# Performance work log

Hardware: AMD Instinct MI355X
Metric: run time of the kernel (lower is better)

Reference implementation:

```python
import jax, jax.numpy as jnp
import numpy as np

SEQ, BATCH = 256, 8
N_NODES = SEQ * BATCH
VOCAB, D_MODEL, H, D_K, D_FF, N_LAYERS, MAX_POS = 259, 256, 8, 32, 1024, 2, 128


def setup_inputs() -> dict:
    key = jax.random.key(0)
    ks = jax.random.split(key, 16)
    # structured causal edge list per sequence (dst attends to src <= dst, incl. self)
    tri_dst, tri_src = np.tril_indices(SEQ)
    offs = (np.arange(BATCH) * SEQ)[:, None]
    edge_src = jnp.asarray((tri_src[None, :] + offs).ravel(), dtype=jnp.int64)
    edge_dst = jnp.asarray((tri_dst[None, :] + offs).ravel(), dtype=jnp.int64)
    positions = jnp.tile(jnp.arange(SEQ, dtype=jnp.int64), BATCH)
    tokens = jax.random.randint(ks[0], (N_NODES,), 0, VOCAB, dtype=jnp.int64)
    s = 0.02
    p = lambda k, shp: jax.random.normal(k, shp, dtype=jnp.float32) * s
    return {
        "tokens": tokens, "positions": positions,
        "edge_src": edge_src, "edge_dst": edge_dst,
        "coord_emb": p(ks[1], (3, D_MODEL)),
        "pos_emb": p(ks[2], (MAX_POS, D_MODEL)),
        "value_emb": p(ks[3], (VOCAB, D_MODEL)),
        "ln1_scale": jnp.ones((N_LAYERS, D_MODEL)), "ln1_bias": jnp.zeros((N_LAYERS, D_MODEL)),
        "Wqkv": p(ks[4], (N_LAYERS, D_MODEL, 3 * D_MODEL)),
        "Wo": p(ks[5], (N_LAYERS, D_MODEL, D_MODEL)),
        "ln2_scale": jnp.ones((N_LAYERS, D_MODEL)), "ln2_bias": jnp.zeros((N_LAYERS, D_MODEL)),
        "W1": p(ks[6], (N_LAYERS, D_MODEL, D_FF)), "b1": jnp.zeros((N_LAYERS, D_FF)),
        "W2": p(ks[7], (N_LAYERS, D_FF, D_MODEL)), "b2": jnp.zeros((N_LAYERS, D_MODEL)),
        "lnf_scale": jnp.ones((D_MODEL,)), "lnf_bias": jnp.zeros((D_MODEL,)),
        "Wg": p(ks[8], (D_MODEL, VOCAB)), "bg": jnp.zeros((VOCAB,)),
    }


def _ln(x, scale, bias, eps=1e-5):
    mu = jnp.mean(x, axis=-1, keepdims=True)
    var = jnp.var(x, axis=-1, keepdims=True)
    return (x - mu) * jax.lax.rsqrt(var + eps) * scale + bias


def _graph_attention(x, src, dst, Wqkv, Wo, ln_s, ln_b):
    n = x.shape[0]
    xn = _ln(x, ln_s, ln_b)
    qkv = (xn @ Wqkv).reshape(n, 3, H, D_K)
    q, k, v = qkv[:, 0], qkv[:, 1], qkv[:, 2]  # [n, H, D_K] each
    # u_dot_v('k','q','score') per edge, scaled
    score = jnp.einsum("ehd,ehd->eh", k[src], q[dst]) / jnp.sqrt(jnp.float32(D_K))
    # edge_softmax over incoming edges of each dst node
    smax = jax.ops.segment_max(score, dst, num_segments=n)      # [n, H]
    ex = jnp.exp(score - smax[dst])                              # [E, H]
    denom = jax.ops.segment_sum(ex, dst, num_segments=n)        # [n, H]
    alpha = ex / denom[dst]
    # u_mul_e('v','softmax_score') + sum reduce -> z on dst nodes
    z = jax.ops.segment_sum(alpha[:, :, None] * v[src], dst, num_segments=n)  # [n, H, D_K]
    return x + z.reshape(n, D_MODEL) @ Wo


def reference(tokens, positions, edge_src, edge_dst, coord_emb, pos_emb, value_emb,
              ln1_scale, ln1_bias, Wqkv, Wo, ln2_scale, ln2_bias, W1, b1, W2, b2,
              lnf_scale, lnf_bias, Wg, bg):
    x = coord_emb[positions % 3] + pos_emb[positions // 3] + value_emb[tokens]
    for i in range(Wqkv.shape[0]):
        x = _graph_attention(x, edge_src, edge_dst, Wqkv[i], Wo[i], ln1_scale[i], ln1_bias[i])
        h = _ln(x, ln2_scale[i], ln2_bias[i])
        x = x + jax.nn.relu(h @ W1[i] + b1[i]) @ W2[i] + b2[i]
    out = _ln(x, lnf_scale, lnf_bias) @ Wg + bg
    return jax.nn.log_softmax(out, axis=-1)
```

## Files before the change

kernel.cpp:

```cpp
#include <hip/hip_runtime.h>
#include <hip/hip_bf16.h>

typedef __hip_bfloat16 bf16;
typedef unsigned short ushort_t;
typedef unsigned int uint_t;
typedef __attribute__((ext_vector_type(8))) short short8;
typedef __attribute__((ext_vector_type(4))) float floatx4;

#define D_MODEL 256
#define SEQ     256
#define BATCH   8
#define NN      2048
#define NHEAD   8
#define DK      32
#define DFF     1024
#define VOCAB   259
#define NLAYER  2

#define WQKVT_OFF 0
#define WOT_OFF   393216
#define W1T_OFF   524288
#define W2T_OFF   1048576
#define WGT_OFF   1572864
#define WT_TOTAL  1639168
// ... 178 lines not shown
    int base = b * SEQ;
    int dstBase = tile * 64;
    int tileEnd = (tile + 1) * 64;

    int nV = tileEnd * 4;
    for (int i = t; i < nV; i += 256) {
        int src = i >> 2, g = i & 3;
        const ushort_t* rp = qkvB + (size_t)(base + src) * 768 + h * 32 + g * 8;
        uint4 kv = *reinterpret_cast<const uint4*>(rp + 256);
        *reinterpret_cast<uint4*>(&u.a.Ks[src][g * 8]) = kv;
        uint4 vv = *reinterpret_cast<const uint4*>(rp + 512);
        const ushort_t* vs = (const ushort_t*)&vv;
        #pragma unroll
        for (int j = 0; j < 8; ++j) Vt[g * 8 + j][src] = vs[j];
    }
    {
        int r = t >> 2, g = t & 3;
        uint4 qv = *reinterpret_cast<const uint4*>(
            qkvB + (size_t)(base + dstBase + r) * 768 + h * 32 + g * 8);
        *reinterpret_cast<uint4*>(&u.a.Qs[r][g * 8]) = qv;
    }
    __syncthreads();

    const float scale = 0.17677669529663687f;
    int stLim = tile * 4 + wave;
    int stCnt = stLim + 1;
    short8 qf = *reinterpret_cast<const short8*>(&u.a.Qs[wave * 16 + l16][quad * 8]);
    floatx4 accs[16];
    #pragma unroll
    for (int st = 0; st < 16; ++st) {
        if (st <= stLim) {
            short8 kf = *reinterpret_cast<const short8*>(&u.a.Ks[st * 16 + l16][quad * 8]);
            accs[st] = __builtin_amdgcn_mfma_f32_16x16x32_bf16(qf, kf, (floatx4){0.f,0.f,0.f,0.f}, 0, 0, 0);
        }
    }
    float mrow[4] = {-3e38f, -3e38f, -3e38f, -3e38f};
    #pragma unroll
    for (int st = 0; st < 16; ++st) {
        if (st <= stLim) {
            int srcg = st * 16 + l16;
            #pragma unroll
            for (int r = 0; r < 4; ++r) {
                int dstg = dstBase + wave * 16 + quad * 4 + r;
                float sv = (srcg <= dstg) ? accs[st][r] * scale : -3e38f;
                accs[st][r] = sv;
                mrow[r] = fmaxf(mrow[r], sv);
            }
        }
    }
    #pragma unroll
    for (int mk = 1; mk < 16; mk <<= 1)
        #pragma unroll
        for (int r = 0; r < 4; ++r) mrow[r] = fmaxf(mrow[r], __shfl_xor(mrow[r], mk, 64));
    float lrow[4] = {0.f, 0.f, 0.f, 0.f};
    #pragma unroll
    for (int st = 0; st < 16; ++st) {
        if (st <= stLim) {
            #pragma unroll
            for (int r = 0; r < 4; ++r) {
                float p = __expf(accs[st][r] - mrow[r]);
                accs[st][r] = p;
                lrow[r] += p;
            }
        }
    }
    #pragma unroll
    for (int mk = 1; mk < 16; mk <<= 1)
        #pragma unroll
        for (int r = 0; r < 4; ++r) lrow[r] += __shfl_xor(lrow[r], mk, 64);
    __syncthreads();

    #pragma unroll
    for (int st = 0; st < 16; ++st) {
        if (st <= stLim) {
            #pragma unroll
            for (int r = 0; r < 4; ++r)
                u.Ps[wave * 16 + quad * 4 + r][st * 16 + l16] = f2bs(accs[st][r]);
        }
    }
    if (stCnt & 1) {
        #pragma unroll
        for (int r = 0; r < 4; ++r)
            u.Ps[wave * 16 + quad * 4 + r][stCnt * 16 + l16] = 0;
    }
    __syncthreads();

    int ktCnt = (stCnt + 1) >> 1;
    floatx4 acco[2];
    acco[0] = (floatx4){0.f,0.f,0.f,0.f};
    acco[1] = (floatx4){0.f,0.f,0.f,0.f};
    #pragma unroll
    for (int kt = 0; kt < 8; ++kt) {
        if (kt < ktCnt) {
            short8 pf = *reinterpret_cast<const short8*>(&u.Ps[wave * 16 + l16][kt * 32 + quad * 8]);
            #pragma unroll
            for (int dn = 0; dn < 2; ++dn) {
                short8 vf = *reinterpret_cast<const short8*>(&Vt[dn * 16 + l16][kt * 32 + quad * 8]);
                acco[dn] = __builtin_amdgcn_mfma_f32_16x16x32_bf16(pf, vf, acco[dn], 0, 0, 0);
            }
        }
    }
    #pragma unroll
    for (int dn = 0; dn < 2; ++dn)
        #pragma unroll
        for (int r = 0; r < 4; ++r)
            zB[(size_t)(base + dstBase + wave * 16 + quad * 4 + r) * 256
               + h * 32 + dn * 16 + l16] = f2bs(acco[dn][r] / lrow[r]);
}

__global__ void __launch_bounds__(256) gemm_k(const ushort_t* __restrict__ A, int K,
        const ushort_t* __restrict__ BT, const float* __restrict__ bias,
        ushort_t* __restrict__ C, int ldc, int relu) {
    int t = threadIdx.x;
    int lane = t & 63, wave = t >> 6;
    int quad = lane >> 4, l16 = lane & 15;
    int wm = (wave >> 1) * 32, wn = (wave & 1) * 32;
    int rowBase = blockIdx.x * 64, colBase = blockIdx.y * 64;
    floatx4 acc[2][2];
    #pragma unroll
    for (int a = 0; a < 2; ++a)
        #pragma unroll
        for (int b = 0; b < 2; ++b) acc[a][b] = (floatx4){0.f,0.f,0.f,0.f};
    const ushort_t* a0 = A + (size_t)(rowBase + wm + l16) * K + quad * 8;
    const ushort_t* a1 = a0 + (size_t)16 * K;
    const ushort_t* b0 = BT + (size_t)(colBase + wn + l16) * K + quad * 8;
    const ushort_t* b1 = b0 + (size_t)16 * K;
    #pragma unroll 8
    for (int k0 = 0; k0 < K; k0 += 32) {
        short8 af0 = *reinterpret_cast<const short8*>(a0 + k0);
        short8 af1 = *reinterpret_cast<const short8*>(a1 + k0);
        short8 bf0 = *reinterpret_cast<const short8*>(b0 + k0);
        short8 bf1 = *reinterpret_cast<const short8*>(b1 + k0);
        acc[0][0] = __builtin_amdgcn_mfma_f32_16x16x32_bf16(af0, bf0, acc[0][0], 0,0,0);
        acc[0][1] = __builtin_amdgcn_mfma_f32_16x16x32_bf16(af0, bf1, acc[0][1], 0,0,0);
        acc[1][0] = __builtin_amdgcn_mfma_f32_16x16x32_bf16(af1, bf0, acc[1][0], 0,0,0);
        acc[1][1] = __builtin_amdgcn_mfma_f32_16x16x32_bf16(af1, bf1, acc[1][1], 0,0,0);
    }
    #pragma unroll
    for (int nt = 0; nt < 2; ++nt) {
        int col = colBase + wn + nt*16 + l16;
        float bb = bias ? bias[col] : 0.f;
        #pragma unroll
        for (int mt = 0; mt < 2; ++mt)
            #pragma unroll
            for (int r = 0; r < 4; ++r) {
                int row = rowBase + wm + mt*16 + quad*4 + r;
                float v = acc[mt][nt][r] + bb;
                if (relu) v = fmaxf(v, 0.f);
                C[(size_t)row * ldc + col] = f2bs(v);
            }
    }
}

union TailHU {
    ushort_t hmid[16][1032];
    float    Lg[16][273];
};

__device__ __forceinline__ void ln16_store(const float (*xrow)[256],
        const float* __restrict__ ls, const float* __restrict__ lb,
        ushort_t (*xnA)[264]) {
    int lane = threadIdx.x & 63, wave = threadIdx.x >> 6;
    #pragma unroll
    for (int i = 0; i < 4; ++i) {
        int row = wave*4 + i, c0 = lane * 4;
        float4 vv = *reinterpret_cast<const float4*>(&xrow[row][c0]);
        float s  = wred_sum(vv.x + vv.y + vv.z + vv.w);
        float s2 = wred_sum(vv.x*vv.x + vv.y*vv.y + vv.z*vv.z + vv.w*vv.w);
        float mu = s * (1.f/256.f);
        float var = s2 * (1.f/256.f) - mu*mu;
        float rstd = rsqrtf(var + 1e-5f);
        ushort4 o;
        o.x = f2bs((vv.x-mu)*rstd*ls[c0+0] + lb[c0+0]);
        o.y = f2bs((vv.y-mu)*rstd*ls[c0+1] + lb[c0+1]);
        o.z = f2bs((vv.z-mu)*rstd*ls[c0+2] + lb[c0+2]);
        o.w = f2bs((vv.w-mu)*rstd*ls[c0+3] + lb[c0+3]);
        *reinterpret_cast<ushort4*>(&xnA[row][c0]) = o;
    }
}

__global__ void __launch_bounds__(256) tail_k(
        const ushort_t* __restrict__ zB,
        const ushort_t* __restrict__ WoT,
        float* __restrict__ x,
        const float* __restrict__ ls2, const float* __restrict__ lb2,
        const ushort_t* __restrict__ W1T, const float* __restrict__ b1P,
        const ushort_t* __restrict__ W2T, const float* __restrict__ b2P,
        const float* __restrict__ lsN, const float* __restrict__ lbN,
        const ushort_t* __restrict__ WqkvTn, ushort_t* __restrict__ qkvB,
        const ushort_t* __restrict__ WgT, const float* __restrict__ bgP,
        const void* __restrict__ ln1sRaw, void* __restrict__ outp, int doLogits) {
    __shared__ ushort_t xnA[16][264];
    __shared__ float    xrow[16][256];
    __shared__ TailHU   hu;
    int t = threadIdx.x, lane = t & 63, wave = t >> 6;
    int quad = lane >> 4, l16 = lane & 15;
    int rowBase = blockIdx.x * 16;
    int cb = wave * 64;
    float vpre[4][4];

    {
        floatx4 acc[4];
        #pragma unroll
        for (int nt = 0; nt < 4; ++nt) acc[nt] = (floatx4){0.f,0.f,0.f,0.f};
        const ushort_t* a0 = zB + (size_t)(rowBase + l16) * 256 + quad * 8;
        #pragma unroll
        for (int k0 = 0; k0 < 256; k0 += 32) {
            short8 af = *reinterpret_cast<const short8*>(a0 + k0);
            #pragma unroll
            for (int nt = 0; nt < 4; ++nt) {
                short8 bv = *reinterpret_cast<const short8*>(
                    WoT + (size_t)(cb + nt*16 + l16) * 256 + k0 + quad * 8);
                acc[nt] = __builtin_amdgcn_mfma_f32_16x16x32_bf16(af, bv, acc[nt], 0,0,0);
            }
        }
        #pragma unroll
        for (int nt = 0; nt < 4; ++nt) {
            int col = cb + nt*16 + l16;
            #pragma unroll
            for (int r = 0; r < 4; ++r) {
                int row = quad*4 + r;
                float v = acc[nt][r] + x[(size_t)(rowBase + row) * 256 + col];
                vpre[nt][r] = v;
                xrow[row][col] = v;
            }
        }
    }
    __syncthreads();
    ln16_store(xrow, ls2, lb2, xnA);
    __syncthreads();

    {
        floatx4 acc[16];
        #pragma unroll
        for (int nt = 0; nt < 16; ++nt) acc[nt] = (floatx4){0.f,0.f,0.f,0.f};
        const ushort_t* a0 = &xnA[l16][quad * 8];
        #pragma unroll
        for (int k0 = 0; k0 < 256; k0 += 32) {
            short8 af = *reinterpret_cast<const short8*>(a0 + k0);
            #pragma unroll
            for (int nt = 0; nt < 16; ++nt) {
                short8 bv = *reinterpret_cast<const short8*>(
                    W1T + (size_t)(wave*256 + nt*16 + l16) * 256 + k0 + quad * 8);
                acc[nt] = __builtin_amdgcn_mfma_f32_16x16x32_bf16(af, bv, acc[nt], 0,0,0);
            }
        }
        #pragma unroll
        for (int nt = 0; nt < 16; ++nt) {
            int col = wave*256 + nt*16 + l16;
            float bb = b1P[col];
            #pragma unroll
            for (int r = 0; r < 4; ++r)
                hu.hmid[quad*4 + r][col] = f2bs(fmaxf(acc[nt][r] + bb, 0.f));
        }
    }
    __syncthreads();

    {
        floatx4 acc[4];
        #pragma unroll
        for (int nt = 0; nt < 4; ++nt) acc[nt] = (floatx4){0.f,0.f,0.f,0.f};
        #pragma unroll 8
        for (int k0 = 0; k0 < 1024; k0 += 32) {
            short8 af = *reinterpret_cast<const short8*>(&hu.hmid[l16][k0 + quad * 8]);
            #pragma unroll
            for (int nt = 0; nt < 4; ++nt) {
                short8 bv = *reinterpret_cast<const short8*>(
                    W2T + (size_t)(cb + nt*16 + l16) * 1024 + k0 + quad * 8);
                acc[nt] = __builtin_amdgcn_mfma_f32_16x16x32_bf16(af, bv, acc[nt], 0,0,0);
            }
        }
        #pragma unroll
        for (int nt = 0; nt < 4; ++nt) {
            int col = cb + nt*16 + l16;
            float bb = b2P[col];
            #pragma unroll
            for (int r = 0; r < 4; ++r) {
                int row = quad*4 + r;
                float v = acc[nt][r] + bb + vpre[nt][r];
                x[(size_t)(rowBase + row) * 256 + col] = v;
                xrow[row][col] = v;
            }
        }
    }
    __syncthreads();
    ln16_store(xrow, lsN, lbN, xnA);
    __syncthreads();

    if (WqkvTn) {
        floatx4 acc[12];
        #pragma unroll
        for (int nt = 0; nt < 12; ++nt) acc[nt] = (floatx4){0.f,0.f,0.f,0.f};
        const ushort_t* a0 = &xnA[l16][quad * 8];
        #pragma unroll
        for (int k0 = 0; k0 < 256; k0 += 32) {
            short8 af = *reinterpret_cast<const short8*>(a0 + k0);
            #pragma unroll
            for (int nt = 0; nt < 12; ++nt) {
                short8 bv = *reinterpret_cast<const short8*>(
                    WqkvTn + (size_t)(wave*192 + nt*16 + l16) * 256 + k0 + quad * 8);
                acc[nt] = __builtin_amdgcn_mfma_f32_16x16x32_bf16(af, bv, acc[nt], 0,0,0);
            }
        }
        #pragma unroll
        for (int nt = 0; nt < 12; ++nt) {
            int col = wave*192 + nt*16 + l16;
            #pragma unroll
            for (int r = 0; r < 4; ++r)
                qkvB[(size_t)(rowBase + quad*4 + r) * 768 + col] = f2bs(acc[nt][r]);
        }
    }

    if (doLogits) {
        const ushort_t* a0 = &xnA[l16][quad * 8];
        {
            floatx4 acc[4];
            #pragma unroll
            for (int nt = 0; nt < 4; ++nt) acc[nt] = (floatx4){0.f,0.f,0.f,0.f};
            #pragma unroll
            for (int kc = 0; kc < 8; ++kc) {
                short8 af = *reinterpret_cast<const short8*>(a0 + kc * 32);
                #pragma unroll
                for (int nt = 0; nt < 4; ++nt) {
                    short8 bv = *reinterpret_cast<const short8*>(
                        WgT + (size_t)(cb + nt*16 + l16) * 256 + kc*32 + quad*8);
                    acc[nt] = __builtin_amdgcn_mfma_f32_16x16x32_bf16(af, bv, acc[nt], 0,0,0);
                }
            }
            #pragma unroll
            for (int nt = 0; nt < 4; ++nt) {
                int col = cb + nt*16 + l16;
                float bb = bgP[col];
                #pragma unroll
                for (int r = 0; r < 4; ++r)
                    hu.Lg[quad*4 + r][col] = acc[nt][r] + bb;
            }
        }
        if (wave == 0) {
            floatx4 acc = (floatx4){0.f,0.f,0.f,0.f};
            int n = 256 + l16;
            int nc = (n < VOCAB) ? n : 0;
            const ushort_t* b0 = WgT + (size_t)nc * 256 + quad * 8;
            #pragma unroll
            for (int kc = 0; kc < 8; ++kc) {
                short8 af = *reinterpret_cast<const short8*>(a0 + kc * 32);
                short8 bv = *reinterpret_cast<const short8*>(b0 + kc * 32);
                acc = __builtin_amdgcn_mfma_f32_16x16x32_bf16(af, bv, acc, 0,0,0);
            }
            #pragma unroll
            for (int r = 0; r < 4; ++r)
                hu.Lg[quad*4 + r][256 + l16] = (n < VOCAB) ? (acc[r] + bgP[n]) : -1e30f;
        }
        __syncthreads();
        int outBF = detBF(ln1sRaw) ? 1 : 0;
        #pragma unroll
        for (int i = 0; i < 4; ++i) {
            int row = wave*4 + i;
            float v0 = hu.Lg[row][lane],     v1 = hu.Lg[row][lane+64];
            float v2 = hu.Lg[row][lane+128], v3 = hu.Lg[row][lane+192];
            float v4 = (lane < 16) ? hu.Lg[row][256+lane] : -1e30f;
            float m = wred_max(fmaxf(fmaxf(fmaxf(v0,v1), fmaxf(v2,v3)), v4));
            float se = __expf(v0-m) + __expf(v1-m) + __expf(v2-m) + __expf(v3-m)
                     + ((lane < 16) ? __expf(v4-m) : 0.f);
            se = wred_sum(se);
            float lse = m + logf(se);
            size_t nbase = (size_t)(rowBase + row) * VOCAB;
            if (outBF) {
                ushort_t* o = (ushort_t*)outp + nbase;
                o[lane]     = f2bs(v0 - lse);
                o[lane+64]  = f2bs(v1 - lse);
                o[lane+128] = f2bs(v2 - lse);
                o[lane+192] = f2bs(v3 - lse);
                if (lane < 3) o[256+lane] = f2bs(v4 - lse);
            } else {
                float* o = (float*)outp + nbase;
                o[lane]     = v0 - lse;
                o[lane+64]  = v1 - lse;
                o[lane+128] = v2 - lse;
                o[lane+192] = v3 - lse;
                if (lane < 3) o[256+lane] = v4 - lse;
            }
        }
    }
}

extern "C" void kernel_launch(void* const* d_in, const int* in_sizes, int n_in,
                              void* d_out, int out_size, void* d_ws, size_t ws_size,
                              hipStream_t stream) {
    const void* tok  = d_in[0];
    const void* pos  = d_in[1];
    const void* ce   = d_in[4];
    const void* pe   = d_in[5];
    const void* ve   = d_in[6];
    const void* ln1s = d_in[7];
    const void* ln1b = d_in[8];
    const void* Wqkv = d_in[9];
    const void* Wo   = d_in[10];
    const void* ln2s = d_in[11];
    const void* ln2b = d_in[12];
    const void* W1   = d_in[13];
    const void* b1   = d_in[14];
    const void* W2   = d_in[15];
    const void* b2   = d_in[16];
    const void* lnfs = d_in[17];
    const void* lnfb = d_in[18];
    const void* Wg   = d_in[19];
    const void* bg   = d_in[20];

    char* base = (char*)d_ws;
    float*    lnP  = (float*)base;
    float*    bP   = (float*)(base + 10240);
    float*    x    = (float*)(base + 22528);
    ushort_t* xn   = (ushort_t*)(base + 2119680);
    ushort_t* zB   = (ushort_t*)(base + 3168256);
    ushort_t* WT   = (ushort_t*)(base + 8411136);
    ushort_t* qkvB = (ushort_t*)(base + 11689472);

    prep_k<<<554, 256, 0, stream>>>(tok, pos, ce, pe, ve,
        Wqkv, Wo, W1, W2, Wg, ln1s, ln1b, ln2s, ln2b, lnfs, lnfb,
        b1, b2, bg, WT, lnP, bP, x, xn);

    gemm_k<<<dim3(32, 12), 256, 0, stream>>>(xn, 256,
        WT + WQKVT_OFF, nullptr, qkvB, 768, 0);

    attn_k<<<256, 256, 0, stream>>>(qkvB, zB);

    tail_k<<<128, 256, 0, stream>>>(zB,
        WT + WOT_OFF, x, lnP + 1024, lnP + 1536,
        WT + W1T_OFF, bP, WT + W2T_OFF, bP + 2048,
        lnP + 256, lnP + 768,
        WT + WQKVT_OFF + 196608, qkvB,
        WT + WGT_OFF, bP + 2560, ln1s, d_out, 0);

    attn_k<<<256, 256, 0, stream>>>(qkvB, zB);

    tail_k<<<128, 256, 0, stream>>>(zB,
        WT + WOT_OFF + 65536, x, lnP + 1024 + 256, lnP + 1536 + 256,
        WT + W1T_OFF + 262144, bP + 1024, WT + W2T_OFF + 262144, bP + 2048 + 256,
        lnP + 2048, lnP + 2304,
        nullptr, qkvB,
        WT + WGT_OFF, bP + 2560, ln1s, d_out, 1);
}
```

Before: 228.6 us.

## Widen tail kernel to 1024 threads, one 16-column tile per wave

The fused tail kernel (Wo projection, LN, FFN, next-layer QKV or logits) goes from 4 waves to 16 waves per 16-row block. Each wave now handles one 16-column output tile instead of four (or a quarter of the previous FFN/QKV columns), and each LN or log-softmax row is handled by one wave. The aim is more waves in flight per block, since only 128 blocks launch and the MFMA chains per wave are long. In exchange, register budget per thread drops under the 1024-thread launch bound, and there is more cross-wave synchronisation per block.

```diff
diff --git a/kernel.cpp b/kernel.cpp
--- a/kernel.cpp
+++ b/kernel.cpp
@@ -362,26 +362,23 @@
 __device__ __forceinline__ void ln16_store(const float (*xrow)[256],
         const float* __restrict__ ls, const float* __restrict__ lb,
         ushort_t (*xnA)[264]) {
-    int lane = threadIdx.x & 63, wave = threadIdx.x >> 6;
-    #pragma unroll
-    for (int i = 0; i < 4; ++i) {
-        int row = wave*4 + i, c0 = lane * 4;
-        float4 vv = *reinterpret_cast<const float4*>(&xrow[row][c0]);
-        float s  = wred_sum(vv.x + vv.y + vv.z + vv.w);
-        float s2 = wred_sum(vv.x*vv.x + vv.y*vv.y + vv.z*vv.z + vv.w*vv.w);
-        float mu = s * (1.f/256.f);
-        float var = s2 * (1.f/256.f) - mu*mu;
-        float rstd = rsqrtf(var + 1e-5f);
-        ushort4 o;
-        o.x = f2bs((vv.x-mu)*rstd*ls[c0+0] + lb[c0+0]);
-        o.y = f2bs((vv.y-mu)*rstd*ls[c0+1] + lb[c0+1]);
-        o.z = f2bs((vv.z-mu)*rstd*ls[c0+2] + lb[c0+2]);
-        o.w = f2bs((vv.w-mu)*rstd*ls[c0+3] + lb[c0+3]);
-        *reinterpret_cast<ushort4*>(&xnA[row][c0]) = o;
-    }
-}
-
-__global__ void __launch_bounds__(256) tail_k(
+    int lane = threadIdx.x & 63, row = threadIdx.x >> 6;
+    int c0 = lane * 4;
+    float4 vv = *reinterpret_cast<const float4*>(&xrow[row][c0]);
+    float s  = wred_sum(vv.x + vv.y + vv.z + vv.w);
+    float s2 = wred_sum(vv.x*vv.x + vv.y*vv.y + vv.z*vv.z + vv.w*vv.w);
+    float mu = s * (1.f/256.f);
+    float var = s2 * (1.f/256.f) - mu*mu;
+    float rstd = rsqrtf(var + 1e-5f);
+    ushort4 o;
+    o.x = f2bs((vv.x-mu)*rstd*ls[c0+0] + lb[c0+0]);
+    o.y = f2bs((vv.y-mu)*rstd*ls[c0+1] + lb[c0+1]);
+    o.z = f2bs((vv.z-mu)*rstd*ls[c0+2] + lb[c0+2]);
+    o.w = f2bs((vv.w-mu)*rstd*ls[c0+3] + lb[c0+3]);
+    *reinterpret_cast<ushort4*>(&xnA[row][c0]) = o;
+}
+
+__global__ void __launch_bounds__(1024) tail_k(
         const ushort_t* __restrict__ zB,
         const ushort_t* __restrict__ WoT,
         float* __restrict__ x,
@@ -398,58 +395,49 @@
     int t = threadIdx.x, lane = t & 63, wave = t >> 6;
     int quad = lane >> 4, l16 = lane & 15;
     int rowBase = blockIdx.x * 16;
-    int cb = wave * 64;
-    float vpre[4][4];
+    float vpre[4];
+
+    {
+        floatx4 acc = (floatx4){0.f,0.f,0.f,0.f};
+        const ushort_t* a0 = zB + (size_t)(rowBase + l16) * 256 + quad * 8;
+        const ushort_t* b0 = WoT + (size_t)(wave*16 + l16) * 256 + quad * 8;
+        #pragma unroll
+        for (int k0 = 0; k0 < 256; k0 += 32) {
+            short8 af = *reinterpret_cast<const short8*>(a0 + k0);
+            short8 bv = *reinterpret_cast<const short8*>(b0 + k0);
+            acc = __builtin_amdgcn_mfma_f32_16x16x32_bf16(af, bv, acc, 0,0,0);
+        }
+        int col = wave*16 + l16;
+        #pragma unroll
+        for (int r = 0; r < 4; ++r) {
+            int row = quad*4 + r;
+            float v = acc[r] + x[(size_t)(rowBase + row) * 256 + col];
+            vpre[r] = v;
+            xrow[row][col] = v;
+        }
+    }
+    __syncthreads();
+    ln16_store(xrow, ls2, lb2, xnA);
+    __syncthreads();
 
     {
         floatx4 acc[4];
         #pragma unroll
         for (int nt = 0; nt < 4; ++nt) acc[nt] = (floatx4){0.f,0.f,0.f,0.f};
-        const ushort_t* a0 = zB + (size_t)(rowBase + l16) * 256 + quad * 8;
+        const ushort_t* a0 = &xnA[l16][quad * 8];
         #pragma unroll
         for (int k0 = 0; k0 < 256; k0 += 32) {
             short8 af = *reinterpret_cast<const short8*>(a0 + k0);
             #pragma unroll
             for (int nt = 0; nt < 4; ++nt) {
                 short8 bv = *reinterpret_cast<const short8*>(
-                    WoT + (size_t)(cb + nt*16 + l16) * 256 + k0 + quad * 8);
+                    W1T + (size_t)(wave*64 + nt*16 + l16) * 256 + k0 + quad * 8);
                 acc[nt] = __builtin_amdgcn_mfma_f32_16x16x32_bf16(af, bv, acc[nt], 0,0,0);
             }
         }
         #pragma unroll
         for (int nt = 0; nt < 4; ++nt) {
-            int col = cb + nt*16 + l16;
-            #pragma unroll
-            for (int r = 0; r < 4; ++r) {
-                int row = quad*4 + r;
-                float v = acc[nt][r] + x[(size_t)(rowBase + row) * 256 + col];
-                vpre[nt][r] = v;
-                xrow[row][col] = v;
-            }
-        }
-    }
-    __syncthreads();
-    ln16_store(xrow, ls2, lb2, xnA);
-    __syncthreads();
-
-    {
-        floatx4 acc[16];
-        #pragma unroll
-        for (int nt = 0; nt < 16; ++nt) acc[nt] = (floatx4){0.f,0.f,0.f,0.f};
-        const ushort_t* a0 = &xnA[l16][quad * 8];
-        #pragma unroll
-        for (int k0 = 0; k0 < 256; k0 += 32) {
-            short8 af = *reinterpret_cast<const short8*>(a0 + k0);
-            #pragma unroll
-            for (int nt = 0; nt < 16; ++nt) {
-                short8 bv = *reinterpret_cast<const short8*>(
-                    W1T + (size_t)(wave*256 + nt*16 + l16) * 256 + k0 + quad * 8);
-                acc[nt] = __builtin_amdgcn_mfma_f32_16x16x32_bf16(af, bv, acc[nt], 0,0,0);
-            }
-        }
-        #pragma unroll
-        for (int nt = 0; nt < 16; ++nt) {
-            int col = wave*256 + nt*16 + l16;
+            int col = wave*64 + nt*16 + l16;
             float bb = b1P[col];
             #pragma unroll
             for (int r = 0; r < 4; ++r)
@@ -459,30 +447,22 @@
     __syncthreads();
 
     {
-        floatx4 acc[4];
-        #pragma unroll
-        for (int nt = 0; nt < 4; ++nt) acc[nt] = (floatx4){0.f,0.f,0.f,0.f};
+        floatx4 acc = (floatx4){0.f,0.f,0.f,0.f};
+        const ushort_t* b0 = W2T + (size_t)(wave*16 + l16) * 1024 + quad * 8;
         #pragma unroll 8
         for (int k0 = 0; k0 < 1024; k0 += 32) {
             short8 af = *reinterpret_cast<const short8*>(&hu.hmid[l16][k0 + quad * 8]);
-            #pragma unroll
-            for (int nt = 0; nt < 4; ++nt) {
-                short8 bv = *reinterpret_cast<const short8*>(
-                    W2T + (size_t)(cb + nt*16 + l16) * 1024 + k0 + quad * 8);
-                acc[nt] = __builtin_amdgcn_mfma_f32_16x16x32_bf16(af, bv, acc[nt], 0,0,0);
-            }
-        }
-        #pragma unroll
-        for (int nt = 0; nt < 4; ++nt) {
-            int col = cb + nt*16 + l16;
-            float bb = b2P[col];
-            #pragma unroll
-            for (int r = 0; r < 4; ++r) {
-                int row = quad*4 + r;
-                float v = acc[nt][r] + bb + vpre[nt][r];
-                x[(size_t)(rowBase + row) * 256 + col] = v;
-                xrow[row][col] = v;
-            }
+            short8 bv = *reinterpret_cast<const short8*>(b0 + k0);
+            acc = __builtin_amdgcn_mfma_f32_16x16x32_bf16(af, bv, acc, 0,0,0);
+        }
+        int col = wave*16 + l16;
+        float bb = b2P[col];
+        #pragma unroll
+        for (int r = 0; r < 4; ++r) {
+            int row = quad*4 + r;
+            float v = acc[r] + bb + vpre[r];
+            x[(size_t)(rowBase + row) * 256 + col] = v;
+            xrow[row][col] = v;
         }
     }
     __syncthreads();
@@ -490,23 +470,23 @@
     __syncthreads();
 
     if (WqkvTn) {
-        floatx4 acc[12];
-        #pragma unroll
-        for (int nt = 0; nt < 12; ++nt) acc[nt] = (floatx4){0.f,0.f,0.f,0.f};
+        floatx4 acc[3];
+        #pragma unroll
+        for (int nt = 0; nt < 3; ++nt) acc[nt] = (floatx4){0.f,0.f,0.f,0.f};
         const ushort_t* a0 = &xnA[l16][quad * 8];
         #pragma unroll
         for (int k0 = 0; k0 < 256; k0 += 32) {
             short8 af = *reinterpret_cast<const short8*>(a0 + k0);
             #pragma unroll
-            for (int nt = 0; nt < 12; ++nt) {
+            for (int nt = 0; nt < 3; ++nt) {
                 short8 bv = *reinterpret_cast<const short8*>(
-                    WqkvTn + (size_t)(wave*192 + nt*16 + l16) * 256 + k0 + quad * 8);
+                    WqkvTn + (size_t)(wave*48 + nt*16 + l16) * 256 + k0 + quad * 8);
                 acc[nt] = __builtin_amdgcn_mfma_f32_16x16x32_bf16(af, bv, acc[nt], 0,0,0);
             }
         }
         #pragma unroll
-        for (int nt = 0; nt < 12; ++nt) {
-            int col = wave*192 + nt*16 + l16;
+        for (int nt = 0; nt < 3; ++nt) {
+            int col = wave*48 + nt*16 + l16;
             #pragma unroll
             for (int r = 0; r < 4; ++r)
                 qkvB[(size_t)(rowBase + quad*4 + r) * 768 + col] = f2bs(acc[nt][r]);
@@ -516,27 +496,19 @@
     if (doLogits) {
         const ushort_t* a0 = &xnA[l16][quad * 8];
         {
-            floatx4 acc[4];
-            #pragma unroll
-            for (int nt = 0; nt < 4; ++nt) acc[nt] = (floatx4){0.f,0.f,0.f,0.f};
+            floatx4 acc = (floatx4){0.f,0.f,0.f,0.f};
+            const ushort_t* b0 = WgT + (size_t)(wave*16 + l16) * 256 + quad * 8;
             #pragma unroll
             for (int kc = 0; kc < 8; ++kc) {
                 short8 af = *reinterpret_cast<const short8*>(a0 + kc * 32);
-                #pragma unroll
-                for (int nt = 0; nt < 4; ++nt) {
-                    short8 bv = *reinterpret_cast<const short8*>(
-                        WgT + (size_t)(cb + nt*16 + l16) * 256 + kc*32 + quad*8);
-                    acc[nt] = __builtin_amdgcn_mfma_f32_16x16x32_bf16(af, bv, acc[nt], 0,0,0);
-                }
-            }
-            #pragma unroll
-            for (int nt = 0; nt < 4; ++nt) {
-                int col = cb + nt*16 + l16;
-                float bb = bgP[col];
-                #pragma unroll
-                for (int r = 0; r < 4; ++r)
-                    hu.Lg[quad*4 + r][col] = acc[nt][r] + bb;
-            }
+                short8 bv = *reinterpret_cast<const short8*>(b0 + kc * 32);
+                acc = __builtin_amdgcn_mfma_f32_16x16x32_bf16(af, bv, acc, 0,0,0);
+            }
+            int col = wave*16 + l16;
+            float bb = bgP[col];
+            #pragma unroll
+            for (int r = 0; r < 4; ++r)
+                hu.Lg[quad*4 + r][col] = acc[r] + bb;
         }
         if (wave == 0) {
             floatx4 acc = (floatx4){0.f,0.f,0.f,0.f};
@@ -555,9 +527,8 @@
         }
         __syncthreads();
         int outBF = detBF(ln1sRaw) ? 1 : 0;
-        #pragma unroll
-        for (int i = 0; i < 4; ++i) {
-            int row = wave*4 + i;
+        {
+            int row = wave;
             float v0 = hu.Lg[row][lane],     v1 = hu.Lg[row][lane+64];
             float v2 = hu.Lg[row][lane+128], v3 = hu.Lg[row][lane+192];
             float v4 = (lane < 16) ? hu.Lg[row][256+lane] : -1e30f;
@@ -627,7 +598,7 @@
 
     attn_k<<<256, 256, 0, stream>>>(qkvB, zB);
 
-    tail_k<<<128, 256, 0, stream>>>(zB,
+    tail_k<<<128, 1024, 0, stream>>>(zB,
         WT + WOT_OFF, x, lnP + 1024, lnP + 1536,
         WT + W1T_OFF, bP, WT + W2T_OFF, bP + 2048,
         lnP + 256, lnP + 768,
@@ -636,7 +607,7 @@
 
     attn_k<<<256, 256, 0, stream>>>(qkvB, zB);
 
-    tail_k<<<128, 256, 0, stream>>>(zB,
+    tail_k<<<128, 1024, 0, stream>>>(zB,
         WT + WOT_OFF + 65536, x, lnP + 1024 + 256, lnP + 1536 + 256,
         WT + W1T_OFF + 262144, bP + 1024, WT + W2T_OFF + 262144, bP + 2048 + 256,
         lnP + 2048, lnP + 2304,
```

New measurement: 229.1 us. About the same (+0.2%).

## Split fused tail kernel into multi-kernel FFN pipeline for more parallelism

Applied to the files above, without the earlier changes.

Replaces the monolithic per-layer tail kernel (128 blocks doing Wo, LN, W1, W2, LN, QKV/logits serially) with four kernels: Wo+LN+W1 on a 64x4 grid, W2 on 64x4, LN+QKV on 32x12, and LN+logits. The goal is to fill the GPU with more blocks, since 128 blocks underuse the CUs. The trade is extra launches, a global round trip for the 2048x1024 hidden activation, and Wo/LN work redone across the 4 column groups. Ping-pong x buffers avoid read/write hazards across blocks.

```diff
diff --git a/kernel.cpp b/kernel.cpp
--- a/kernel.cpp
+++ b/kernel.cpp
@@ -354,19 +354,153 @@
     }
 }
 
-union TailHU {
-    ushort_t hmid[16][1032];
-    float    Lg[16][273];
-};
-
-__device__ __forceinline__ void ln16_store(const float (*xrow)[256],
+__global__ void __launch_bounds__(256) woff1_k(
+        const ushort_t* __restrict__ zB, const ushort_t* __restrict__ WoT,
+        const float* __restrict__ xIn, float* __restrict__ xOut,
+        const float* __restrict__ ls2, const float* __restrict__ lb2,
+        const ushort_t* __restrict__ W1T, const float* __restrict__ b1P,
+        ushort_t* __restrict__ hmidG) {
+    __shared__ float    xrow[32][256];
+    __shared__ ushort_t xnA[32][264];
+    int t = threadIdx.x, lane = t & 63, wave = t >> 6;
+    int quad = lane >> 4, l16 = lane & 15;
+    int rowBase = blockIdx.x * 32, cg = blockIdx.y;
+
+    {
+        floatx4 acc[2][4];
+        #pragma unroll
+        for (int mt = 0; mt < 2; ++mt)
+            #pragma unroll
+            for (int nt = 0; nt < 4; ++nt) acc[mt][nt] = (floatx4){0.f,0.f,0.f,0.f};
+        const ushort_t* a0 = zB + (size_t)(rowBase + l16) * 256 + quad * 8;
+        const ushort_t* a1 = a0 + (size_t)16 * 256;
+        #pragma unroll
+        for (int k0 = 0; k0 < 256; k0 += 32) {
+            short8 af0 = *reinterpret_cast<const short8*>(a0 + k0);
+            short8 af1 = *reinterpret_cast<const short8*>(a1 + k0);
+            #pragma unroll
+            for (int nt = 0; nt < 4; ++nt) {
+                short8 bv = *reinterpret_cast<const short8*>(
+                    WoT + (size_t)(wave*64 + nt*16 + l16) * 256 + k0 + quad * 8);
+                acc[0][nt] = __builtin_amdgcn_mfma_f32_16x16x32_bf16(af0, bv, acc[0][nt], 0,0,0);
+                acc[1][nt] = __builtin_amdgcn_mfma_f32_16x16x32_bf16(af1, bv, acc[1][nt], 0,0,0);
+            }
+        }
+        #pragma unroll
+        for (int nt = 0; nt < 4; ++nt) {
+            int col = wave*64 + nt*16 + l16;
+            #pragma unroll
+            for (int mt = 0; mt < 2; ++mt)
+                #pragma unroll
+                for (int r = 0; r < 4; ++r) {
+                    int row = mt*16 + quad*4 + r;
+                    float v = acc[mt][nt][r] + xIn[(size_t)(rowBase + row) * 256 + col];
+                    xOut[(size_t)(rowBase + row) * 256 + col] = v;
+                    xrow[row][col] = v;
+                }
+        }
+    }
+    __syncthreads();
+    #pragma unroll
+    for (int i = 0; i < 8; ++i) {
+        int row = wave*8 + i, c0 = lane * 4;
+        float4 vv = *reinterpret_cast<const float4*>(&xrow[row][c0]);
+        float s  = wred_sum(vv.x + vv.y + vv.z + vv.w);
+        float s2 = wred_sum(vv.x*vv.x + vv.y*vv.y + vv.z*vv.z + vv.w*vv.w);
+        float mu = s * (1.f/256.f);
+        float var = s2 * (1.f/256.f) - mu*mu;
+        float rstd = rsqrtf(var + 1e-5f);
+        ushort4 o;
+        o.x = f2bs((vv.x-mu)*rstd*ls2[c0+0] + lb2[c0+0]);
+        o.y = f2bs((vv.y-mu)*rstd*ls2[c0+1] + lb2[c0+1]);
+        o.z = f2bs((vv.z-mu)*rstd*ls2[c0+2] + lb2[c0+2]);
+        o.w = f2bs((vv.w-mu)*rstd*ls2[c0+3] + lb2[c0+3]);
+        *reinterpret_cast<ushort4*>(&xnA[row][c0]) = o;
+    }
+    __syncthreads();
+    {
+        floatx4 acc[2][4];
+        #pragma unroll
+        for (int mt = 0; mt < 2; ++mt)
+            #pragma unroll
+            for (int nt = 0; nt < 4; ++nt) acc[mt][nt] = (floatx4){0.f,0.f,0.f,0.f};
+        const ushort_t* a0 = &xnA[l16][quad * 8];
+        const ushort_t* a1 = &xnA[16 + l16][quad * 8];
+        #pragma unroll
+        for (int k0 = 0; k0 < 256; k0 += 32) {
+            short8 af0 = *reinterpret_cast<const short8*>(a0 + k0);
+            short8 af1 = *reinterpret_cast<const short8*>(a1 + k0);
+            #pragma unroll
+            for (int nt = 0; nt < 4; ++nt) {
+                short8 bv = *reinterpret_cast<const short8*>(
+                    W1T + (size_t)(cg*256 + wave*64 + nt*16 + l16) * 256 + k0 + quad * 8);
+                acc[0][nt] = __builtin_amdgcn_mfma_f32_16x16x32_bf16(af0, bv, acc[0][nt], 0,0,0);
+                acc[1][nt] = __builtin_amdgcn_mfma_f32_16x16x32_bf16(af1, bv, acc[1][nt], 0,0,0);
+            }
+        }
+        #pragma unroll
+        for (int nt = 0; nt < 4; ++nt) {
+            int col = cg*256 + wave*64 + nt*16 + l16;
+            float bb = b1P[col];
+            #pragma unroll
+            for (int mt = 0; mt < 2; ++mt)
+                #pragma unroll
+                for (int r = 0; r < 4; ++r) {
+                    int row = mt*16 + quad*4 + r;
+                    hmidG[(size_t)(rowBase + row) * 1024 + col] =
+                        f2bs(fmaxf(acc[mt][nt][r] + bb, 0.f));
+                }
+        }
+    }
+}
+
+__global__ void __launch_bounds__(256) w2_k(
+        const ushort_t* __restrict__ hmidG, const ushort_t* __restrict__ W2T,
+        const float* __restrict__ b2P,
+        const float* __restrict__ xPre, float* __restrict__ yOut) {
+    int t = threadIdx.x, lane = t & 63, wave = t >> 6;
+    int quad = lane >> 4, l16 = lane & 15;
+    int rowBase = blockIdx.x * 32, colBase = blockIdx.y * 64;
+    int wm = (wave >> 1) * 16, wn = (wave & 1) * 32;
+    floatx4 acc[2];
+    acc[0] = (floatx4){0.f,0.f,0.f,0.f};
+    acc[1] = (floatx4){0.f,0.f,0.f,0.f};
+    const ushort_t* a0 = hmidG + (size_t)(rowBase + wm + l16) * 1024 + quad * 8;
+    #pragma unroll 8
+    for (int k0 = 0; k0 < 1024; k0 += 32) {
+        short8 af = *reinterpret_cast<const short8*>(a0 + k0);
+        #pragma unroll
+        for (int nt = 0; nt < 2; ++nt) {
+            short8 bv = *reinterpret_cast<const short8*>(
+                W2T + (size_t)(colBase + wn + nt*16 + l16) * 1024 + k0 + quad * 8);
+            acc[nt] = __builtin_amdgcn_mfma_f32_16x16x32_bf16(af, bv, acc[nt], 0,0,0);
+        }
+    }
+    #pragma unroll
+    for (int nt = 0; nt < 2; ++nt) {
+        int col = colBase + wn + nt*16 + l16;
+        float bb = b2P[col];
+        #pragma unroll
+        for (int r = 0; r < 4; ++r) {
+            int row = wm + quad*4 + r;
+            float v = acc[nt][r] + bb + xPre[(size_t)(rowBase + row) * 256 + col];
+            yOut[(size_t)(rowBase + row) * 256 + col] = v;
+        }
+    }
+}
+
+__global__ void __launch_bounds__(256) lnqkv_k(
+        const float* __restrict__ yIn,
         const float* __restrict__ ls, const float* __restrict__ lb,
-        ushort_t (*xnA)[264]) {
-    int lane = threadIdx.x & 63, wave = threadIdx.x >> 6;
-    #pragma unroll
-    for (int i = 0; i < 4; ++i) {
-        int row = wave*4 + i, c0 = lane * 4;
-        float4 vv = *reinterpret_cast<const float4*>(&xrow[row][c0]);
+        const ushort_t* __restrict__ WqkvT, ushort_t* __restrict__ qkvB) {
+    __shared__ ushort_t xnA[64][264];
+    int t = threadIdx.x, lane = t & 63, wave = t >> 6;
+    int quad = lane >> 4, l16 = lane & 15;
+    int rowBase = blockIdx.x * 64, colBase = blockIdx.y * 64;
+    #pragma unroll
+    for (int i = 0; i < 16; ++i) {
+        int row = wave*16 + i, c0 = lane * 4;
+        float4 vv = *reinterpret_cast<const float4*>(yIn + (size_t)(rowBase + row) * 256 + c0);
         float s  = wred_sum(vv.x + vv.y + vv.z + vv.w);
         float s2 = wred_sum(vv.x*vv.x + vv.y*vv.y + vv.z*vv.z + vv.w*vv.w);
         float mu = s * (1.f/256.f);
@@ -379,209 +513,144 @@
         o.w = f2bs((vv.w-mu)*rstd*ls[c0+3] + lb[c0+3]);
         *reinterpret_cast<ushort4*>(&xnA[row][c0]) = o;
     }
-}
-
-__global__ void __launch_bounds__(256) tail_k(
-        const ushort_t* __restrict__ zB,
-        const ushort_t* __restrict__ WoT,
-        float* __restrict__ x,
-        const float* __restrict__ ls2, const float* __restrict__ lb2,
-        const ushort_t* __restrict__ W1T, const float* __restrict__ b1P,
-        const ushort_t* __restrict__ W2T, const float* __restrict__ b2P,
-        const float* __restrict__ lsN, const float* __restrict__ lbN,
-        const ushort_t* __restrict__ WqkvTn, ushort_t* __restrict__ qkvB,
+    __syncthreads();
+    int wm = (wave >> 1) * 32, wn = (wave & 1) * 32;
+    floatx4 acc[2][2];
+    #pragma unroll
+    for (int a = 0; a < 2; ++a)
+        #pragma unroll
+        for (int b = 0; b < 2; ++b) acc[a][b] = (floatx4){0.f,0.f,0.f,0.f};
+    const ushort_t* a0 = &xnA[wm + l16][quad * 8];
+    const ushort_t* a1 = &xnA[wm + 16 + l16][quad * 8];
+    #pragma unroll
+    for (int k0 = 0; k0 < 256; k0 += 32) {
+        short8 af0 = *reinterpret_cast<const short8*>(a0 + k0);
+        short8 af1 = *reinterpret_cast<const short8*>(a1 + k0);
+        #pragma unroll
+        for (int nt = 0; nt < 2; ++nt) {
+            short8 bv = *reinterpret_cast<const short8*>(
+                WqkvT + (size_t)(colBase + wn + nt*16 + l16) * 256 + k0 + quad * 8);
+            acc[0][nt] = __builtin_amdgcn_mfma_f32_16x16x32_bf16(af0, bv, acc[0][nt], 0,0,0);
+            acc[1][nt] = __builtin_amdgcn_mfma_f32_16x16x32_bf16(af1, bv, acc[1][nt], 0,0,0);
+        }
+    }
+    #pragma unroll
+    for (int nt = 0; nt < 2; ++nt) {
+        int col = colBase + wn + nt*16 + l16;
+        #pragma unroll
+        for (int mt = 0; mt < 2; ++mt)
+            #pragma unroll
+            for (int r = 0; r < 4; ++r) {
+                int row = wm + mt*16 + quad*4 + r;
+                qkvB[(size_t)(rowBase + row) * 768 + col] = f2bs(acc[mt][nt][r]);
+            }
+    }
+}
+
+__global__ void __launch_bounds__(256) lnlg_k(
+        const float* __restrict__ yIn,
+        const float* __restrict__ lnfsP, const float* __restrict__ lnfbP,
         const ushort_t* __restrict__ WgT, const float* __restrict__ bgP,
-        const void* __restrict__ ln1sRaw, void* __restrict__ outp, int doLogits) {
+        const void* __restrict__ ln1sRaw, void* __restrict__ outp) {
+    __shared__ float    xrow[16][256];
     __shared__ ushort_t xnA[16][264];
-    __shared__ float    xrow[16][256];
-    __shared__ TailHU   hu;
+    __shared__ float    Lg[16][273];
     int t = threadIdx.x, lane = t & 63, wave = t >> 6;
     int quad = lane >> 4, l16 = lane & 15;
     int rowBase = blockIdx.x * 16;
+    #pragma unroll
+    for (int i = 0; i < 4; ++i) {
+        int idx = i * 256 + t;
+        int row = idx >> 6, c4 = (idx & 63) * 4;
+        *reinterpret_cast<float4*>(&xrow[row][c4]) =
+            *reinterpret_cast<const float4*>(yIn + (size_t)(rowBase + row) * 256 + c4);
+    }
+    __syncthreads();
+    #pragma unroll
+    for (int i = 0; i < 4; ++i) {
+        int row = wave*4 + i, c0 = lane * 4;
+        float4 vv = *reinterpret_cast<const float4*>(&xrow[row][c0]);
+        float s  = wred_sum(vv.x + vv.y + vv.z + vv.w);
+        float s2 = wred_sum(vv.x*vv.x + vv.y*vv.y + vv.z*vv.z + vv.w*vv.w);
+        float mu = s * (1.f/256.f);
+        float var = s2 * (1.f/256.f) - mu*mu;
+        float rstd = rsqrtf(var + 1e-5f);
+        ushort4 o;
+        o.x = f2bs((vv.x-mu)*rstd*lnfsP[c0+0] + lnfbP[c0+0]);
+        o.y = f2bs((vv.y-mu)*rstd*lnfsP[c0+1] + lnfbP[c0+1]);
+        o.z = f2bs((vv.z-mu)*rstd*lnfsP[c0+2] + lnfbP[c0+2]);
+        o.w = f2bs((vv.w-mu)*rstd*lnfsP[c0+3] + lnfbP[c0+3]);
+        *reinterpret_cast<ushort4*>(&xnA[row][c0]) = o;
+    }
+    __syncthreads();
+    const ushort_t* a0 = &xnA[l16][quad * 8];
     int cb = wave * 64;
-    float vpre[4][4];
-
     {
         floatx4 acc[4];
         #pragma unroll
         for (int nt = 0; nt < 4; ++nt) acc[nt] = (floatx4){0.f,0.f,0.f,0.f};
-        const ushort_t* a0 = zB + (size_t)(rowBase + l16) * 256 + quad * 8;
-        #pragma unroll
-        for (int k0 = 0; k0 < 256; k0 += 32) {
-            short8 af = *reinterpret_cast<const short8*>(a0 + k0);
+        #pragma unroll
+        for (int kc = 0; kc < 8; ++kc) {
+            short8 af = *reinterpret_cast<const short8*>(a0 + kc * 32);
             #pragma unroll
             for (int nt = 0; nt < 4; ++nt) {
                 short8 bv = *reinterpret_cast<const short8*>(
-                    WoT + (size_t)(cb + nt*16 + l16) * 256 + k0 + quad * 8);
+                    WgT + (size_t)(cb + nt*16 + l16) * 256 + kc*32 + quad*8);
                 acc[nt] = __builtin_amdgcn_mfma_f32_16x16x32_bf16(af, bv, acc[nt], 0,0,0);
             }
         }
         #pragma unroll
         for (int nt = 0; nt < 4; ++nt) {
             int col = cb + nt*16 + l16;
-            #pragma unroll
-            for (int r = 0; r < 4; ++r) {
-                int row = quad*4 + r;
-                float v = acc[nt][r] + x[(size_t)(rowBase + row) * 256 + col];
-                vpre[nt][r] = v;
-                xrow[row][col] = v;
-            }
-        }
-    }
-    __syncthreads();
-    ln16_store(xrow, ls2, lb2, xnA);
-    __syncthreads();
-
-    {
-        floatx4 acc[16];
-        #pragma unroll
-        for (int nt = 0; nt < 16; ++nt) acc[nt] = (floatx4){0.f,0.f,0.f,0.f};
-        const ushort_t* a0 = &xnA[l16][quad * 8];
-        #pragma unroll
-        for (int k0 = 0; k0 < 256; k0 += 32) {
-            short8 af = *reinterpret_cast<const short8*>(a0 + k0);
-            #pragma unroll
-            for (int nt = 0; nt < 16; ++nt) {
-                short8 bv = *reinterpret_cast<const short8*>(
-                    W1T + (size_t)(wave*256 + nt*16 + l16) * 256 + k0 + quad * 8);
-                acc[nt] = __builtin_amdgcn_mfma_f32_16x16x32_bf16(af, bv, acc[nt], 0,0,0);
-            }
-        }
-        #pragma unroll
-        for (int nt = 0; nt < 16; ++nt) {
-            int col = wave*256 + nt*16 + l16;
-            float bb = b1P[col];
+            float bb = bgP[col];
             #pragma unroll
             for (int r = 0; r < 4; ++r)
-                hu.hmid[quad*4 + r][col] = f2bs(fmaxf(acc[nt][r] + bb, 0.f));
-        }
-    }
-    __syncthreads();
-
-    {
-        floatx4 acc[4];
-        #pragma unroll
-        for (int nt = 0; nt < 4; ++nt) acc[nt] = (floatx4){0.f,0.f,0.f,0.f};
-        #pragma unroll 8
-        for (int k0 = 0; k0 < 1024; k0 += 32) {
-            short8 af = *reinterpret_cast<const short8*>(&hu.hmid[l16][k0 + quad * 8]);
-            #pragma unroll
-            for (int nt = 0; nt < 4; ++nt) {
-                short8 bv = *reinterpret_cast<const short8*>(
-                    W2T + (size_t)(cb + nt*16 + l16) * 1024 + k0 + quad * 8);
-                acc[nt] = __builtin_amdgcn_mfma_f32_16x16x32_bf16(af, bv, acc[nt], 0,0,0);
-            }
-        }
-        #pragma unroll
-        for (int nt = 0; nt < 4; ++nt) {
-            int col = cb + nt*16 + l16;
-            float bb = b2P[col];
-            #pragma unroll
-            for (int r = 0; r < 4; ++r) {
-                int row = quad*4 + r;
-                float v = acc[nt][r] + bb + vpre[nt][r];
-                x[(size_t)(rowBase + row) * 256 + col] = v;
-                xrow[row][col] = v;
-            }
-        }
-    }
-    __syncthreads();
-    ln16_store(xrow, lsN, lbN, xnA);
-    __syncthreads();
-
-    if (WqkvTn) {
-        floatx4 acc[12];
-        #pragma unroll
-        for (int nt = 0; nt < 12; ++nt) acc[nt] = (floatx4){0.f,0.f,0.f,0.f};
-        const ushort_t* a0 = &xnA[l16][quad * 8];
-        #pragma unroll
-        for (int k0 = 0; k0 < 256; k0 += 32) {
-            short8 af = *reinterpret_cast<const short8*>(a0 + k0);
-            #pragma unroll
-            for (int nt = 0; nt < 12; ++nt) {
-                short8 bv = *reinterpret_cast<const short8*>(
-                    WqkvTn + (size_t)(wave*192 + nt*16 + l16) * 256 + k0 + quad * 8);
-                acc[nt] = __builtin_amdgcn_mfma_f32_16x16x32_bf16(af, bv, acc[nt], 0,0,0);
-            }
-        }
-        #pragma unroll
-        for (int nt = 0; nt < 12; ++nt) {
-            int col = wave*192 + nt*16 + l16;
-            #pragma unroll
-            for (int r = 0; r < 4; ++r)
-                qkvB[(size_t)(rowBase + quad*4 + r) * 768 + col] = f2bs(acc[nt][r]);
-        }
-    }
-
-    if (doLogits) {
-        const ushort_t* a0 = &xnA[l16][quad * 8];
-        {
-            floatx4 acc[4];
-            #pragma unroll
-            for (int nt = 0; nt < 4; ++nt) acc[nt] = (floatx4){0.f,0.f,0.f,0.f};
-            #pragma unroll
-            for (int kc = 0; kc < 8; ++kc) {
-                short8 af = *reinterpret_cast<const short8*>(a0 + kc * 32);
-                #pragma unroll
-                for (int nt = 0; nt < 4; ++nt) {
-                    short8 bv = *reinterpret_cast<const short8*>(
-                        WgT + (size_t)(cb + nt*16 + l16) * 256 + kc*32 + quad*8);
-                    acc[nt] = __builtin_amdgcn_mfma_f32_16x16x32_bf16(af, bv, acc[nt], 0,0,0);
-                }
-            }
-            #pragma unroll
-            for (int nt = 0; nt < 4; ++nt) {
-                int col = cb + nt*16 + l16;
-                float bb = bgP[col];
-                #pragma unroll
-                for (int r = 0; r < 4; ++r)
-                    hu.Lg[quad*4 + r][col] = acc[nt][r] + bb;
-            }
-        }
-        if (wave == 0) {
-            floatx4 acc = (floatx4){0.f,0.f,0.f,0.f};
-            int n = 256 + l16;
-            int nc = (n < VOCAB) ? n : 0;
-            const ushort_t* b0 = WgT + (size_t)nc * 256 + quad * 8;
-            #pragma unroll
-            for (int kc = 0; kc < 8; ++kc) {
-                short8 af = *reinterpret_cast<const short8*>(a0 + kc * 32);
-                short8 bv = *reinterpret_cast<const short8*>(b0 + kc * 32);
-                acc = __builtin_amdgcn_mfma_f32_16x16x32_bf16(af, bv, acc, 0,0,0);
-            }
-            #pragma unroll
-            for (int r = 0; r < 4; ++r)
-                hu.Lg[quad*4 + r][256 + l16] = (n < VOCAB) ? (acc[r] + bgP[n]) : -1e30f;
-        }
-        __syncthreads();
-        int outBF = detBF(ln1sRaw) ? 1 : 0;
-        #pragma unroll
-        for (int i = 0; i < 4; ++i) {
-            int row = wave*4 + i;
-            float v0 = hu.Lg[row][lane],     v1 = hu.Lg[row][lane+64];
-            float v2 = hu.Lg[row][lane+128], v3 = hu.Lg[row][lane+192];
-            float v4 = (lane < 16) ? hu.Lg[row][256+lane] : -1e30f;
-            float m = wred_max(fmaxf(fmaxf(fmaxf(v0,v1), fmaxf(v2,v3)), v4));
-            float se = __expf(v0-m) + __expf(v1-m) + __expf(v2-m) + __expf(v3-m)
-                     + ((lane < 16) ? __expf(v4-m) : 0.f);
-            se = wred_sum(se);
-            float lse = m + logf(se);
-            size_t nbase = (size_t)(rowBase + row) * VOCAB;
-            if (outBF) {
-                ushort_t* o = (ushort_t*)outp + nbase;
-                o[lane]     = f2bs(v0 - lse);
-                o[lane+64]  = f2bs(v1 - lse);
-                o[lane+128] = f2bs(v2 - lse);
-                o[lane+192] = f2bs(v3 - lse);
-                if (lane < 3) o[256+lane] = f2bs(v4 - lse);
-            } else {
-                float* o = (float*)outp + nbase;
-                o[lane]     = v0 - lse;
-                o[lane+64]  = v1 - lse;
-                o[lane+128] = v2 - lse;
-                o[lane+192] = v3 - lse;
-                if (lane < 3) o[256+lane] = v4 - lse;
-            }
+                Lg[quad*4 + r][col] = acc[nt][r] + bb;
+        }
+    }
+    if (wave == 0) {
+        floatx4 acc = (floatx4){0.f,0.f,0.f,0.f};
+        int n = 256 + l16;
+        int nc = (n < VOCAB) ? n : 0;
+        const ushort_t* b0 = WgT + (size_t)nc * 256 + quad * 8;
+        #pragma unroll
+        for (int kc = 0; kc < 8; ++kc) {
+            short8 af = *reinterpret_cast<const short8*>(a0 + kc * 32);
+            short8 bv = *reinterpret_cast<const short8*>(b0 + kc * 32);
+            acc = __builtin_amdgcn_mfma_f32_16x16x32_bf16(af, bv, acc, 0,0,0);
+        }
+        #pragma unroll
+        for (int r = 0; r < 4; ++r)
+            Lg[quad*4 + r][256 + l16] = (n < VOCAB) ? (acc[r] + bgP[n]) : -1e30f;
+    }
+    __syncthreads();
+    int outBF = detBF(ln1sRaw) ? 1 : 0;
+    #pragma unroll
+    for (int i = 0; i < 4; ++i) {
+        int row = wave*4 + i;
+        float v0 = Lg[row][lane],     v1 = Lg[row][lane+64];
+        float v2 = Lg[row][lane+128], v3 = Lg[row][lane+192];
+        float v4 = (lane < 16) ? Lg[row][256+lane] : -1e30f;
+        float m = wred_max(fmaxf(fmaxf(fmaxf(v0,v1), fmaxf(v2,v3)), v4));
+        float se = __expf(v0-m) + __expf(v1-m) + __expf(v2-m) + __expf(v3-m)
+                 + ((lane < 16) ? __expf(v4-m) : 0.f);
+        se = wred_sum(se);
+        float lse = m + logf(se);
+        size_t nbase = (size_t)(rowBase + row) * VOCAB;
+        if (outBF) {
+            ushort_t* o = (ushort_t*)outp + nbase;
+            o[lane]     = f2bs(v0 - lse);
+            o[lane+64]  = f2bs(v1 - lse);
+            o[lane+128] = f2bs(v2 - lse);
+            o[lane+192] = f2bs(v3 - lse);
+            if (lane < 3) o[256+lane] = f2bs(v4 - lse);
+        } else {
+            float* o = (float*)outp + nbase;
+            o[lane]     = v0 - lse;
+            o[lane+64]  = v1 - lse;
+            o[lane+128] = v2 - lse;
+            o[lane+192] = v3 - lse;
+            if (lane < 3) o[256+lane] = v4 - lse;
         }
     }
 }
@@ -610,36 +679,40 @@
     const void* bg   = d_in[20];
 
     char* base = (char*)d_ws;
-    float*    lnP  = (float*)base;
-    float*    bP   = (float*)(base + 10240);
-    float*    x    = (float*)(base + 22528);
-    ushort_t* xn   = (ushort_t*)(base + 2119680);
-    ushort_t* zB   = (ushort_t*)(base + 3168256);
-    ushort_t* WT   = (ushort_t*)(base + 8411136);
-    ushort_t* qkvB = (ushort_t*)(base + 11689472);
+    float*    lnP   = (float*)base;
+    float*    bP    = (float*)(base + 10240);
+    float*    xA    = (float*)(base + 22528);
+    ushort_t* xn    = (ushort_t*)(base + 2119680);
+    ushort_t* zB    = (ushort_t*)(base + 3168256);
+    ushort_t* hmidG = (ushort_t*)(base + 4216832);
+    ushort_t* WT    = (ushort_t*)(base + 8411136);
+    ushort_t* qkvB  = (ushort_t*)(base + 11689472);
+    float*    xB    = (float*)(base + 14835200);
+    float*    xC    = (float*)(base + 16932352);
 
     prep_k<<<554, 256, 0, stream>>>(tok, pos, ce, pe, ve,
         Wqkv, Wo, W1, W2, Wg, ln1s, ln1b, ln2s, ln2b, lnfs, lnfb,
-        b1, b2, bg, WT, lnP, bP, x, xn);
+        b1, b2, bg, WT, lnP, bP, xA, xn);
 
     gemm_k<<<dim3(32, 12), 256, 0, stream>>>(xn, 256,
         WT + WQKVT_OFF, nullptr, qkvB, 768, 0);
 
     attn_k<<<256, 256, 0, stream>>>(qkvB, zB);
 
-    tail_k<<<128, 256, 0, stream>>>(zB,
-        WT + WOT_OFF, x, lnP + 1024, lnP + 1536,
-        WT + W1T_OFF, bP, WT + W2T_OFF, bP + 2048,
-        lnP + 256, lnP + 768,
-        WT + WQKVT_OFF + 196608, qkvB,
-        WT + WGT_OFF, bP + 2560, ln1s, d_out, 0);
+    woff1_k<<<dim3(64, 4), 256, 0, stream>>>(zB, WT + WOT_OFF, xA, xB,
+        lnP + 1024, lnP + 1536, WT + W1T_OFF, bP, hmidG);
+    w2_k<<<dim3(64, 4), 256, 0, stream>>>(hmidG, WT + W2T_OFF, bP + 2048, xB, xC);
+
+    lnqkv_k<<<dim3(32, 12), 256, 0, stream>>>(xC, lnP + 256, lnP + 768,
+        WT + WQKVT_OFF + 196608, qkvB);
 
     attn_k<<<256, 256, 0, stream>>>(qkvB, zB);
 
-    tail_k<<<128, 256, 0, stream>>>(zB,
-        WT + WOT_OFF + 65536, x, lnP + 1024 + 256, lnP + 1536 + 256,
-        WT + W1T_OFF + 262144, bP + 1024, WT + W2T_OFF + 262144, bP + 2048 + 256,
-        lnP + 2048, lnP + 2304,
-        nullptr, qkvB,
-        WT + WGT_OFF, bP + 2560, ln1s, d_out, 1);
-}
+    woff1_k<<<dim3(64, 4), 256, 0, stream>>>(zB, WT + WOT_OFF + 65536, xC, xA,
+        lnP + 1024 + 256, lnP + 1536 + 256, WT + W1T_OFF + 262144, bP + 1024, hmidG);
+    w2_k<<<dim3(64, 4), 256, 0, stream>>>(hmidG, WT + W2T_OFF + 262144,
+        bP + 2048 + 256, xA, xB);
+
+    lnlg_k<<<128, 256, 0, stream>>>(xB, lnP + 2048, lnP + 2304,
+        WT + WGT_OFF, bP + 2560, ln1s, d_out);
+}
```

Result: faster. 212.0 us (-7.2%).
